# Kernel tuning notes

Measured on AMD Instinct MI355X. Metric: run time of the kernel, lower is better.

## Reference

```python
import jax, jax.numpy as jnp
import numpy as np

B = 131072
SD, AD, HID = 24, 8, 32
NH = SD + AD            # n_heads = 32
UNITS = HID * NH        # 1024


def _xavier(k, shape):
    fan_in, fan_out = shape[-2], shape[-1]
    lim = float(np.sqrt(6.0 / (fan_in + fan_out)))
    return jax.random.uniform(k, shape, jnp.float32, -lim, lim)


def setup_inputs() -> dict:
    key = jax.random.key(0)
    ks = jax.random.split(key, 8)
    return dict(
        state=jax.random.normal(ks[0], (B, SD), jnp.float32),
        action=jax.random.normal(ks[1], (B, AD), jnp.float32),
        # ripple layer 1: per-head Linear(NH -> HID), gate logits init 0 (init_prob=0.5)
        W1=_xavier(ks[2], (NH, NH, HID)), b1=jnp.zeros((NH, HID), jnp.float32), g1=jnp.zeros((NH,), jnp.float32),
        # ripple layer 2: per-head Linear(UNITS -> HID)
        W2=_xavier(ks[3], (NH, UNITS, HID)), b2=jnp.zeros((NH, HID), jnp.float32), g2=jnp.zeros((NH,), jnp.float32),
        # q_network
        Wq1=_xavier(ks[4], (UNITS, 256)), bq1=jnp.zeros((256,), jnp.float32),
        ln1_g=jnp.ones((256,), jnp.float32), ln1_b=jnp.zeros((256,), jnp.float32),
        Wq2=_xavier(ks[5], (256, 128)), bq2=jnp.zeros((128,), jnp.float32),
        ln2_g=jnp.ones((128,), jnp.float32), ln2_b=jnp.zeros((128,), jnp.float32),
        Wq3=_xavier(ks[6], (128, 1)), bq3=jnp.zeros((1,), jnp.float32),
    )


def _ripple(x, W, b, g):
    # x: [B, D]; W: [H, D, K]; per-head linear + tanh, scaled by per-head sigmoid gate
    h = jnp.tanh(jnp.einsum('bd,hdk->bhk', x, W) + b[None])  # [B, H, K]
    h = h * jax.nn.sigmoid(g)[None, :, None]
    return h.reshape(x.shape[0], -1)  # [B, H*K]


def _ln(x, g, b, eps=1e-5):
    mu = jnp.mean(x, -1, keepdims=True)
    var = jnp.mean((x - mu) ** 2, -1, keepdims=True)
    return (x - mu) * jax.lax.rsqrt(var + eps) * g + b


def reference(state, action, W1, b1, g1, W2, b2, g2,
              Wq1, bq1, ln1_g, ln1_b, Wq2, bq2, ln2_g, ln2_b, Wq3, bq3):
    sa = jnp.concatenate([state, action], axis=1)          # [B, SD+AD]
    x = _ripple(sa, W1, b1, g1)                            # [B, UNITS]
    x = _ripple(x, W2, b2, g2)                             # [B, UNITS]
    h = jax.nn.relu(_ln(x @ Wq1 + bq1, ln1_g, ln1_b))      # [B, 256] (dropout = eval identity)
    h = jax.nn.relu(_ln(h @ Wq2 + bq2, ln2_g, ln2_b))      # [B, 128]
    return h @ Wq3 + bq3                                   # [B, 1]
```

## Files before the change

kernel.cpp:

```cpp
#include <hip/hip_runtime.h>
#include <hip/hip_bf16.h>

typedef _Float16 f16x8 __attribute__((ext_vector_type(8)));
typedef _Float16 f16x4 __attribute__((ext_vector_type(4)));
typedef float f32x4 __attribute__((ext_vector_type(4)));

__device__ __forceinline__ float tanh_fast(float x) {
  float e = __expf(2.0f * x);
  return 1.0f - 2.0f * __builtin_amdgcn_rcpf(e + 1.0f);
}
__device__ __forceinline__ float sigmoid_fast(float x) {
  return __builtin_amdgcn_rcpf(1.0f + __expf(-x));
}

__global__ __launch_bounds__(256) void prep_weights(
    const float* __restrict__ W1, const float* __restrict__ W2,
    const float* __restrict__ Wq1, const float* __restrict__ Wq2,
    _Float16* __restrict__ V1p, _Float16* __restrict__ V2p,
    _Float16* __restrict__ T1p, _Float16* __restrict__ T2p) {
  __shared__ float S[32 * 33];
  int b = blockIdx.x, t = threadIdx.x;
  if (b < 2624) {
    const float* in; _Float16* out; int N, nc0, tile;
    if (b < 2048) {
      int h = b >> 6, rem = b & 63, ntl = rem >> 5, kt = rem & 31;
      in = W2 + (size_t)h * 32768 + (size_t)kt * 32 * 32;
      N = 32; nc0 = ntl * 16;
      out = V2p; tile = kt * 64 + (h * 2 + ntl);
    } else if (b < 2560) {
      int i = b - 2048, nt = i >> 5, kt = i & 31;
      in = Wq1 + (size_t)kt * 32 * 256; N = 256; nc0 = nt * 16;
      out = T1p; tile = kt * 16 + nt;
    } else {
      int i = b - 2560, nt = i >> 3, kt = i & 7;
      in = Wq2 + (size_t)kt * 32 * 128; N = 128; nc0 = nt * 16;
      out = T2p; tile = nt * 8 + kt;
    }
    if (t < 128) {
      int r = t >> 2, c4 = (t & 3) * 4;
      const float4 v = *(const float4*)(in + (size_t)r * N + nc0 + c4);
      S[r * 17 + c4 + 0] = v.x; S[r * 17 + c4 + 1] = v.y;
      S[r * 17 + c4 + 2] = v.z; S[r * 17 + c4 + 3] = v.w;
    }
    __syncthreads();
    if (t < 128) {
      int w2 = t >> 6, l = t & 63, q = l >> 4, l15 = l & 15;
      f16x4 o;
#pragma unroll
      for (int jj = 0; jj < 4; ++jj)
        o[jj] = (_Float16)S[(q * 8 + w2 * 4 + jj) * 17 + l15];
      *(f16x4*)(out + (size_t)tile * 512 + l * 8 + w2 * 4) = o;
    }
  } else {
    int h = b - 2624;
    const float* in = W1 + h * 1024;
    int cc = t & 31, rr8 = t >> 5;
#pragma unroll
    for (int p = 0; p < 4; ++p) {
      int r = rr8 + p * 8;
      S[cc * 33 + r] = in[r * 32 + cc];
    }
    __syncthreads();
    if (t < 128) {
      int ntl = t >> 6, l = t & 63, q = l >> 4, l15 = l & 15;
      f16x8 o;
#pragma unroll
      for (int j = 0; j < 8; ++j)
        o[j] = (_Float16)S[(ntl * 16 + l15) * 33 + q * 8 + j];
      *(f16x8*)(V1p + (size_t)(h * 2 + ntl) * 512 + l * 8) = o;
    }
  }
}

__global__ __launch_bounds__(512, 2) void k12_fused(
    const float* __restrict__ state, const float* __restrict__ action,
    const _Float16* __restrict__ v1p, const float* __restrict__ b1,
    const float* __restrict__ g1,
    const _Float16* __restrict__ v2p, const float* __restrict__ b2,
    const float* __restrict__ g2,
    _Float16* __restrict__ x2p, int gro, int NRT) {
  __shared__ __align__(16) _Float16 SA[128 * 40];
  __shared__ __align__(16) _Float16 XF[2 * 16384];
  __shared__ __align__(16) _Float16 EP[8 * 64 * 36];
  int g = blockIdx.x;
  int bn = g & 1, bm = g >> 1;
  int t = threadIdx.x, w = t >> 6, l = t & 63, q = l >> 4, l15 = l & 15;
  int wrow = w & 1;
  int cg = w >> 1;
  int m0 = bm * 128;

  {
    int r = t >> 2, q4 = t & 3;
    size_t grow = (size_t)(gro + m0 + r);
    float v[8];
    if (q4 < 3) {
      const float4* sp = (const float4*)(state + grow * 24 + q4 * 8);
      ((float4*)v)[0] = sp[0]; ((float4*)v)[1] = sp[1];
    } else {
      const float4* ap = (const float4*)(action + grow * 8);
      ((float4*)v)[0] = ap[0]; ((float4*)v)[1] = ap[1];
    }
    f16x8 h0;
#pragma unroll
    for (int j = 0; j < 8; ++j) h0[j] = (_Float16)v[j];
    *(f16x8*)&SA[r * 40 + q4 * 8] = h0;
  }
  __syncthreads();

  f32x4 acc[4][8] = {};
  _Float16* EPw = EP + w * (64 * 36);

  f16x8 rb[2];
#pragma unroll
  for (int ni = 0; ni < 2; ++ni)
    rb[ni] = *(const f16x8*)(v1p + (size_t)(cg * 2 + ni) * 512 + l * 8);

  const int nt0 = bn * 32 + cg * 8;
  const _Float16* bBase = v2p + (size_t)nt0 * 512 + (size_t)l * 8;

  for (int kc = 0; kc < 8; ++kc) {
    f16x8 asa[4];
#pragma unroll
    for (int mi = 0; mi < 4; ++mi)
      asa[mi] = *(const f16x8*)&SA[(wrow * 64 + mi * 16 + l15) * 40 + q * 8];
    f32x4 a1[4][2] = {};
#pragma unroll
    for (int mi = 0; mi < 4; ++mi)
#pragma unroll
      for (int ni = 0; ni < 2; ++ni)
        a1[mi][ni] = __builtin_amdgcn_mfma_f32_16x16x32_f16(asa[mi], rb[ni], a1[mi][ni], 0, 0, 0);
#pragma unroll
    for (int ni = 0; ni < 2; ++ni) {
      int col = kc * 128 + cg * 32 + ni * 16 + l15;
      float sg = sigmoid_fast(g1[col >> 5]);
      float bias = b1[col];
#pragma unroll
      for (int mi = 0; mi < 4; ++mi)
#pragma unroll
        for (int r = 0; r < 4; ++r)
          EPw[(mi * 16 + q * 4 + r) * 36 + ni * 16 + l15] =
              (_Float16)(tanh_fast(a1[mi][ni][r] + bias) * sg);
    }
    _Float16* buf = XF + (kc & 1) * 16384;
#pragma unroll
    for (int rtl = 0; rtl < 4; ++rtl) {
      int base = (rtl * 16 + l15) * 36 + q * 8;
      union { f16x8 v; f16x4 h[2]; } u;
      u.h[0] = *(const f16x4*)&EPw[base];
      u.h[1] = *(const f16x4*)&EPw[base + 4];
      *(f16x8*)(buf + ((cg * 8 + wrow * 4 + rtl) * 64 + l) * 8) = u.v;
    }
    __syncthreads();

    if (kc < 7) {
#pragma unroll
      for (int ni = 0; ni < 2; ++ni)
        rb[ni] = *(const f16x8*)(v1p + (size_t)((kc + 1) * 8 + cg * 2 + ni) * 512 + l * 8);
    }
    int ktg = kc * 4;
    f16x8 bb0[8], bb1[8];
#pragma unroll
    for (int ni = 0; ni < 8; ++ni)
      bb0[ni] = *(const f16x8*)(bBase + (size_t)(ktg * 64 + ni) * 512);
#pragma unroll
    for (int ni = 0; ni < 8; ++ni)
      bb1[ni] = *(const f16x8*)(bBase + (size_t)((ktg + 1) * 64 + ni) * 512);
#pragma unroll
    for (int ktL = 0; ktL < 4; ++ktL) {
      f16x8 af[4];
#pragma unroll
      for (int mi = 0; mi < 4; ++mi)
        af[mi] = *(const f16x8*)(buf + ((ktL * 8 + wrow * 4 + mi) * 64 + l) * 8);
      f16x8* bb = (ktL & 1) ? bb1 : bb0;
#pragma unroll
      for (int mi = 0; mi < 4; ++mi)
#pragma unroll
        for (int ni = 0; ni < 8; ++ni)
          acc[mi][ni] = __builtin_amdgcn_mfma_f32_16x16x32_f16(af[mi], bb[ni], acc[mi][ni], 0, 0, 0);
      if (ktL == 0) {
#pragma unroll
        for (int ni = 0; ni < 8; ++ni)
          bb0[ni] = *(const f16x8*)(bBase + (size_t)((ktg + 2) * 64 + ni) * 512);
      } else if (ktL == 1) {
#pragma unroll
        for (int ni = 0; ni < 8; ++ni)
          bb1[ni] = *(const f16x8*)(bBase + (size_t)((ktg + 3) * 64 + ni) * 512);
      }
    }
  }

  for (int kcg = 0; kcg < 4; ++kcg) {
#pragma unroll
    for (int np = 0; np < 2; ++np) {
      int ni = kcg * 2 + np;
      int col = (nt0 + ni) * 16 + l15;
      float sg = sigmoid_fast(g2[col >> 5]);
      float bias = b2[col];
#pragma unroll
      for (int mi = 0; mi < 4; ++mi)
#pragma unroll
        for (int r = 0; r < 4; ++r)
          EPw[(mi * 16 + q * 4 + r) * 36 + np * 16 + l15] =
              (_Float16)(tanh_fast(acc[mi][ni][r] + bias) * sg);
    }
#pragma unroll
    for (int rtl = 0; rtl < 4; ++rtl) {
      int base = (rtl * 16 + l15) * 36 + q * 8;
      union { f16x8 v; f16x4 h[2]; } u;
      u.h[0] = *(const f16x4*)&EPw[base];
      u.h[1] = *(const f16x4*)&EPw[base + 4];
      int kc2 = (nt0 >> 1) + kcg;
      int rt = bm * 8 + wrow * 4 + rtl;
      *(f16x8*)(x2p + ((size_t)kc2 * NRT + rt) * 512 + l * 8) = u.v;
    }
  }
}

__global__ __launch_bounds__(512, 3) void k3_head(
    const _Float16* __restrict__ x2p, const _Float16* __restrict__ t1p,
    const _Float16* __restrict__ t2p,
    const float* __restrict__ bq1, const float* __restrict__ ln1g, const float* __restrict__ ln1b,
    const float* __restrict__ bq2, const float* __restrict__ ln2g, const float* __restrict__ ln2b,
    const float* __restrict__ wq3, const float* __restrict__ bq3,
    float* __restrict__ out, int NRT, int SROWS) {
  __shared__ __align__(16) _Float16 y1h[128 * 264];
  __shared__ float redA[128 * 4], redB[128 * 4];
  __shared__ float meanv[128], rstdv[128];
  int bm = blockIdx.x;
  int t = threadIdx.x, w = t >> 6, l = t & 63, q = l >> 4, l15 = l & 15;
  int wr = w >> 2, wc = w & 3;

  int gt = bm * 8;
  int slice = 0;
  if (gt >= NRT) { slice = 1; gt -= NRT; }
  int rt0 = gt + wr * 4;

  f32x4 acc[4][4] = {};
  const size_t aStep = (size_t)NRT * 512;
  const _Float16* aP = x2p + (size_t)slice * SROWS * 1024 + (size_t)rt0 * 512 + (size_t)l * 8;
  const _Float16* bP = t1p + (size_t)(wc * 4) * 512 + (size_t)l * 8;

  f16x8 a0[4], a1[4], b0[4], b1[4];
#pragma unroll
  for (int mi = 0; mi < 4; ++mi) a0[mi] = *(const f16x8*)(aP + mi * 512);
#pragma unroll
  for (int ni = 0; ni < 4; ++ni) b0[ni] = *(const f16x8*)(bP + ni * 512);
#pragma unroll
  for (int mi = 0; mi < 4; ++mi) a1[mi] = *(const f16x8*)(aP + aStep + mi * 512);
#pragma unroll
  for (int ni = 0; ni < 4; ++ni) b1[ni] = *(const f16x8*)(bP + 8192 + ni * 512);
  aP += 2 * aStep; bP += 16384;

  for (int kt = 0; kt < 32; kt += 2) {
#pragma unroll
    for (int mi = 0; mi < 4; ++mi)
#pragma unroll
      for (int ni = 0; ni < 4; ++ni)
        acc[mi][ni] = __builtin_amdgcn_mfma_f32_16x16x32_f16(a0[mi], b0[ni], acc[mi][ni], 0, 0, 0);
    if (kt < 30) {
#pragma unroll
      for (int mi = 0; mi < 4; ++mi) a0[mi] = *(const f16x8*)(aP + mi * 512);
#pragma unroll
      for (int ni = 0; ni < 4; ++ni) b0[ni] = *(const f16x8*)(bP + ni * 512);
    }
#pragma unroll
    for (int mi = 0; mi < 4; ++mi)
#pragma unroll
      for (int ni = 0; ni < 4; ++ni)
        acc[mi][ni] = __builtin_amdgcn_mfma_f32_16x16x32_f16(a1[mi], b1[ni], acc[mi][ni], 0, 0, 0);
    if (kt < 30) {
#pragma unroll
      for (int mi = 0; mi < 4; ++mi) a1[mi] = *(const f16x8*)(aP + aStep + mi * 512);
#pragma unroll
      for (int ni = 0; ni < 4; ++ni) b1[ni] = *(const f16x8*)(bP + 8192 + ni * 512);
      aP += 2 * aStep; bP += 16384;
    }
  }

#pragma unroll
  for (int ni = 0; ni < 4; ++ni) {
    int col = wc * 64 + ni * 16 + l15;
    float b = bq1[col];
#pragma unroll
    for (int mi = 0; mi < 4; ++mi)
#pragma unroll
      for (int r = 0; r < 4; ++r) acc[mi][ni][r] += b;
  }
#pragma unroll
  for (int mi = 0; mi < 4; ++mi)
#pragma unroll
    for (int r = 0; r < 4; ++r) {
      int row = wr * 64 + mi * 16 + q * 4 + r;
      float s = 0.f, sq = 0.f;
#pragma unroll
      for (int ni = 0; ni < 4; ++ni) { float v = acc[mi][ni][r]; s += v; sq += v * v; }
#pragma unroll
      for (int off = 1; off < 16; off <<= 1) { s += __shfl_xor(s, off); sq += __shfl_xor(sq, off); }
      if (l15 == 0) { redA[row * 4 + wc] = s; redB[row * 4 + wc] = sq; }
    }
  __syncthreads();
  if (t < 128) {
    float s  = redA[t * 4] + redA[t * 4 + 1] + redA[t * 4 + 2] + redA[t * 4 + 3];
    float sq = redB[t * 4] + redB[t * 4 + 1] + redB[t * 4 + 2] + redB[t * 4 + 3];
    float mean = s * (1.0f / 256.0f);
    float var = sq * (1.0f / 256.0f) - mean * mean;
    meanv[t] = mean; rstdv[t] = rsqrtf(var + 1e-5f);
  }
  __syncthreads();
#pragma unroll
  for (int mi = 0; mi < 4; ++mi)
#pragma unroll
    for (int ni = 0; ni < 4; ++ni)
#pragma unroll
      for (int r = 0; r < 4; ++r) {
        int row = wr * 64 + mi * 16 + q * 4 + r;
        int col = wc * 64 + ni * 16 + l15;
        float y = (acc[mi][ni][r] - meanv[row]) * rstdv[row] * ln1g[col] + ln1b[col];
        y = fmaxf(y, 0.f);
        y1h[row * 264 + col] = (_Float16)y;
      }
  __syncthreads();

  f32x4 a2[4][2] = {};
  for (int kt = 0; kt < 8; ++kt) {
    f16x8 af2[4];
#pragma unroll
    for (int mi = 0; mi < 4; ++mi)
      af2[mi] = *(const f16x8*)&y1h[(wr * 64 + mi * 16 + l15) * 264 + kt * 32 + q * 8];
#pragma unroll
    for (int ni = 0; ni < 2; ++ni) {
      f16x8 bf = *(const f16x8*)(t2p + (size_t)(wc * 2 + ni) * 4096 + kt * 512 + l * 8);
#pragma unroll
      for (int mi = 0; mi < 4; ++mi)
        a2[mi][ni] = __builtin_amdgcn_mfma_f32_16x16x32_f16(af2[mi], bf, a2[mi][ni], 0, 0, 0);
    }
  }
#pragma unroll
  for (int ni = 0; ni < 2; ++ni) {
    int col = wc * 32 + ni * 16 + l15;
    float b = bq2[col];
#pragma unroll
    for (int mi = 0; mi < 4; ++mi)
#pragma unroll
      for (int r = 0; r < 4; ++r) a2[mi][ni][r] += b;
  }
  __syncthreads();
#pragma unroll
  for (int mi = 0; mi < 4; ++mi)
#pragma unroll
    for (int r = 0; r < 4; ++r) {
      int row = wr * 64 + mi * 16 + q * 4 + r;
      float s = 0.f, sq = 0.f;
#pragma unroll
      for (int ni = 0; ni < 2; ++ni) { float v = a2[mi][ni][r]; s += v; sq += v * v; }
#pragma unroll
      for (int off = 1; off < 16; off <<= 1) { s += __shfl_xor(s, off); sq += __shfl_xor(sq, off); }
      if (l15 == 0) { redA[row * 4 + wc] = s; redB[row * 4 + wc] = sq; }
    }
  __syncthreads();
  if (t < 128) {
    float s  = redA[t * 4] + redA[t * 4 + 1] + redA[t * 4 + 2] + redA[t * 4 + 3];
    float sq = redB[t * 4] + redB[t * 4 + 1] + redB[t * 4 + 2] + redB[t * 4 + 3];
    float mean = s * (1.0f / 128.0f);
    float var = sq * (1.0f / 128.0f) - mean * mean;
    meanv[t] = mean; rstdv[t] = rsqrtf(var + 1e-5f);
  }
  __syncthreads();
#pragma unroll
  for (int mi = 0; mi < 4; ++mi)
#pragma unroll
    for (int r = 0; r < 4; ++r) {
      int row = wr * 64 + mi * 16 + q * 4 + r;
      float pr = 0.f;
#pragma unroll
      for (int ni = 0; ni < 2; ++ni) {
        int col = wc * 32 + ni * 16 + l15;
        float y = (a2[mi][ni][r] - meanv[row]) * rstdv[row] * ln2g[col] + ln2b[col];
        y = fmaxf(y, 0.f);
        pr += y * wq3[col];
      }
#pragma unroll
      for (int off = 1; off < 16; off <<= 1) pr += __shfl_xor(pr, off);
      if (l15 == 0) redA[row * 4 + wc] = pr;
    }
  __syncthreads();
  if (t < 128)
    out[bm * 128 + t] = redA[t * 4] + redA[t * 4 + 1] + redA[t * 4 + 2] + redA[t * 4 + 3] + bq3[0];
}

extern "C" void kernel_launch(void* const* d_in, const int* in_sizes, int n_in,
                              void* d_out, int out_size, void* d_ws, size_t ws_size,
                              hipStream_t stream) {
  const float* state  = (const float*)d_in[0];
  const float* action = (const float*)d_in[1];
  const float* W1  = (const float*)d_in[2];
  const float* b1  = (const float*)d_in[3];
  const float* g1  = (const float*)d_in[4];
  const float* W2  = (const float*)d_in[5];
  const float* b2  = (const float*)d_in[6];
  const float* g2  = (const float*)d_in[7];
  const float* Wq1 = (const float*)d_in[8];
  const float* bq1 = (const float*)d_in[9];
  const float* ln1g = (const float*)d_in[10];
  const float* ln1b = (const float*)d_in[11];
  const float* Wq2 = (const float*)d_in[12];
  const float* bq2 = (const float*)d_in[13];
  const float* ln2g = (const float*)d_in[14];
  const float* ln2b = (const float*)d_in[15];
  const float* Wq3 = (const float*)d_in[16];
  const float* bq3 = (const float*)d_in[17];
  int B = in_sizes[0] / 24;

  char* ws = (char*)d_ws;
  _Float16* V1p = (_Float16*)(ws);
  _Float16* V2p = (_Float16*)(ws + 65536);
  _Float16* T1p = (_Float16*)(ws + 65536 + 2097152);
  _Float16* T2p = (_Float16*)(ws + 65536 + 2097152 + 524288);
  size_t woff = (65536 + 2097152 + 524288 + 65536 + 4095) & ~(size_t)4095;

  size_t avail = ws_size > woff ? ws_size - woff : 0;
  int S, G;
  if (avail >= (size_t)32768 * 2048 * 2) {
    S = 32768; G = 2;
  } else {
    long rows = (long)(avail / 2048);
    if (rows > 32768) rows = 32768;
    rows &= ~127L;
    if (rows < 128) rows = 128;
    S = (int)rows; G = 1;
  }
  _Float16* x2 = (_Float16*)(ws + woff);
  int NRT = S / 16;

  prep_weights<<<2656, 256, 0, stream>>>(W1, W2, Wq1, Wq2, V1p, V2p, T1p, T2p);

  int nsl = (B + S - 1) / S;
  for (int i = 0; i < nsl; ++i) {
    int r0 = i * S;
    int Sc = S < (B - r0) ? S : (B - r0);
    int nbm = Sc / 128;
    k12_fused<<<dim3(2 * nbm), 512, 0, stream>>>(state, action, V1p, b1, g1,
                                                 V2p, b2, g2,
                                                 x2 + (size_t)(i % G) * S * 1024, r0, NRT);
    if (i % G == G - 1 || i == nsl - 1) {
      int gstart = (i - i % G) * S;
      int nrows = r0 + Sc - gstart;
      k3_head<<<dim3(nrows / 128), 512, 0, stream>>>(x2, T1p, T2p, bq1, ln1g, ln1b,
                                                     bq2, ln2g, ln2b, Wq3, bq3,
                                                     (float*)d_out + gstart, NRT, S);
    }
  }
}
```

Baseline: 608.5 us.

## Swap MFMA operand order to write epilogue fragments directly, dropping EP staging

Swaps the MFMA A/B operands so each lane's accumulator holds four consecutive K indices of one row. This lets tanh/gate epilogue results be packed straight into f16x8 operand fragments, with no LDS transpose through a staging buffer. The weight prep kernel permutes K order within the V2p and T1p tiles to match the new fragment layout. The EP shared buffer is removed, which shrinks LDS use and cuts LDS round trips. The SA fragments are also hoisted out of the kc loop. This depends on the K permutation being consistent between producer and consumer, including in the unseen k3_head for T1p.

```diff
diff --git a/kernel.cpp b/kernel.cpp
--- a/kernel.cpp
+++ b/kernel.cpp
@@ -21,20 +21,20 @@
   __shared__ float S[32 * 33];
   int b = blockIdx.x, t = threadIdx.x;
   if (b < 2624) {
-    const float* in; _Float16* out; int N, nc0, tile;
+    const float* in; _Float16* out; int N, nc0, tile, use_pi;
     if (b < 2048) {
       int h = b >> 6, rem = b & 63, ntl = rem >> 5, kt = rem & 31;
       in = W2 + (size_t)h * 32768 + (size_t)kt * 32 * 32;
       N = 32; nc0 = ntl * 16;
-      out = V2p; tile = kt * 64 + (h * 2 + ntl);
+      out = V2p; tile = kt * 64 + (h * 2 + ntl); use_pi = 1;
     } else if (b < 2560) {
       int i = b - 2048, nt = i >> 5, kt = i & 31;
       in = Wq1 + (size_t)kt * 32 * 256; N = 256; nc0 = nt * 16;
-      out = T1p; tile = kt * 16 + nt;
+      out = T1p; tile = kt * 16 + nt; use_pi = 1;
     } else {
       int i = b - 2560, nt = i >> 3, kt = i & 7;
       in = Wq2 + (size_t)kt * 32 * 128; N = 128; nc0 = nt * 16;
-      out = T2p; tile = nt * 8 + kt;
+      out = T2p; tile = nt * 8 + kt; use_pi = 0;
     }
     if (t < 128) {
       int r = t >> 2, c4 = (t & 3) * 4;
@@ -47,8 +47,10 @@
       int w2 = t >> 6, l = t & 63, q = l >> 4, l15 = l & 15;
       f16x4 o;
 #pragma unroll
-      for (int jj = 0; jj < 4; ++jj)
-        o[jj] = (_Float16)S[(q * 8 + w2 * 4 + jj) * 17 + l15];
+      for (int jj = 0; jj < 4; ++jj) {
+        int kl = use_pi ? (q * 4 + jj + w2 * 16) : (q * 8 + w2 * 4 + jj);
+        o[jj] = (_Float16)S[kl * 17 + l15];
+      }
       *(f16x4*)(out + (size_t)tile * 512 + l * 8 + w2 * 4) = o;
     }
   } else {
@@ -81,7 +83,6 @@
     _Float16* __restrict__ x2p, int gro, int NRT) {
   __shared__ __align__(16) _Float16 SA[128 * 40];
   __shared__ __align__(16) _Float16 XF[2 * 16384];
-  __shared__ __align__(16) _Float16 EP[8 * 64 * 36];
   int g = blockIdx.x;
   int bn = g & 1, bm = g >> 1;
   int t = threadIdx.x, w = t >> 6, l = t & 63, q = l >> 4, l15 = l & 15;
@@ -107,8 +108,10 @@
   }
   __syncthreads();
 
-  f32x4 acc[4][8] = {};
-  _Float16* EPw = EP + w * (64 * 36);
+  f16x8 asa[4];
+#pragma unroll
+  for (int p = 0; p < 4; ++p)
+    asa[p] = *(const f16x8*)&SA[((wrow * 4 + p) * 16 + l15) * 40 + q * 8];
 
   f16x8 rb[2];
 #pragma unroll
@@ -117,66 +120,54 @@
 
   const int nt0 = bn * 32 + cg * 8;
   const _Float16* bBase = v2p + (size_t)nt0 * 512 + (size_t)l * 8;
+  f32x4 acc[4][8] = {};
 
   for (int kc = 0; kc < 8; ++kc) {
-    f16x8 asa[4];
-#pragma unroll
-    for (int mi = 0; mi < 4; ++mi)
-      asa[mi] = *(const f16x8*)&SA[(wrow * 64 + mi * 16 + l15) * 40 + q * 8];
-    f32x4 a1[4][2] = {};
-#pragma unroll
-    for (int mi = 0; mi < 4; ++mi)
-#pragma unroll
-      for (int ni = 0; ni < 2; ++ni)
-        a1[mi][ni] = __builtin_amdgcn_mfma_f32_16x16x32_f16(asa[mi], rb[ni], a1[mi][ni], 0, 0, 0);
-#pragma unroll
-    for (int ni = 0; ni < 2; ++ni) {
-      int col = kc * 128 + cg * 32 + ni * 16 + l15;
-      float sg = sigmoid_fast(g1[col >> 5]);
-      float bias = b1[col];
-#pragma unroll
-      for (int mi = 0; mi < 4; ++mi)
-#pragma unroll
-        for (int r = 0; r < 4; ++r)
-          EPw[(mi * 16 + q * 4 + r) * 36 + ni * 16 + l15] =
-              (_Float16)(tanh_fast(a1[mi][ni][r] + bias) * sg);
-    }
+    int ktg = kc * 4;
+    f16x8 bb0[8], bb1[8];
+#pragma unroll
+    for (int ni = 0; ni < 8; ++ni)
+      bb0[ni] = *(const f16x8*)(bBase + (size_t)(ktg * 64 + ni) * 512);
+#pragma unroll
+    for (int ni = 0; ni < 8; ++ni)
+      bb1[ni] = *(const f16x8*)(bBase + (size_t)((ktg + 1) * 64 + ni) * 512);
+
     _Float16* buf = XF + (kc & 1) * 16384;
-#pragma unroll
-    for (int rtl = 0; rtl < 4; ++rtl) {
-      int base = (rtl * 16 + l15) * 36 + q * 8;
-      union { f16x8 v; f16x4 h[2]; } u;
-      u.h[0] = *(const f16x4*)&EPw[base];
-      u.h[1] = *(const f16x4*)&EPw[base + 4];
-      *(f16x8*)(buf + ((cg * 8 + wrow * 4 + rtl) * 64 + l) * 8) = u.v;
+    float sg1 = sigmoid_fast(g1[kc * 4 + cg]);
+    f32x4 bs0 = *(const f32x4*)(b1 + kc * 128 + cg * 32 + q * 4);
+    f32x4 bs1 = *(const f32x4*)(b1 + kc * 128 + cg * 32 + 16 + q * 4);
+#pragma unroll
+    for (int p = 0; p < 4; ++p) {
+      f32x4 d0 = {}, d1 = {};
+      d0 = __builtin_amdgcn_mfma_f32_16x16x32_f16(rb[0], asa[p], d0, 0, 0, 0);
+      d1 = __builtin_amdgcn_mfma_f32_16x16x32_f16(rb[1], asa[p], d1, 0, 0, 0);
+      f16x8 o;
+#pragma unroll
+      for (int r = 0; r < 4; ++r) {
+        o[r]     = (_Float16)(tanh_fast(d0[r] + bs0[r]) * sg1);
+        o[4 + r] = (_Float16)(tanh_fast(d1[r] + bs1[r]) * sg1);
+      }
+      *(f16x8*)(buf + (size_t)(cg * 8 + wrow * 4 + p) * 512 + l * 8) = o;
     }
     __syncthreads();
-
     if (kc < 7) {
 #pragma unroll
       for (int ni = 0; ni < 2; ++ni)
         rb[ni] = *(const f16x8*)(v1p + (size_t)((kc + 1) * 8 + cg * 2 + ni) * 512 + l * 8);
     }
-    int ktg = kc * 4;
-    f16x8 bb0[8], bb1[8];
-#pragma unroll
-    for (int ni = 0; ni < 8; ++ni)
-      bb0[ni] = *(const f16x8*)(bBase + (size_t)(ktg * 64 + ni) * 512);
-#pragma unroll
-    for (int ni = 0; ni < 8; ++ni)
-      bb1[ni] = *(const f16x8*)(bBase + (size_t)((ktg + 1) * 64 + ni) * 512);
+
 #pragma unroll
     for (int ktL = 0; ktL < 4; ++ktL) {
-      f16x8 af[4];
+      f16x8 xa[4];
 #pragma unroll
       for (int mi = 0; mi < 4; ++mi)
-        af[mi] = *(const f16x8*)(buf + ((ktL * 8 + wrow * 4 + mi) * 64 + l) * 8);
+        xa[mi] = *(const f16x8*)(buf + (size_t)(ktL * 8 + wrow * 4 + mi) * 512 + l * 8);
       f16x8* bb = (ktL & 1) ? bb1 : bb0;
 #pragma unroll
       for (int mi = 0; mi < 4; ++mi)
 #pragma unroll
         for (int ni = 0; ni < 8; ++ni)
-          acc[mi][ni] = __builtin_amdgcn_mfma_f32_16x16x32_f16(af[mi], bb[ni], acc[mi][ni], 0, 0, 0);
+          acc[mi][ni] = __builtin_amdgcn_mfma_f32_16x16x32_f16(bb[ni], xa[mi], acc[mi][ni], 0, 0, 0);
       if (ktL == 0) {
 #pragma unroll
         for (int ni = 0; ni < 8; ++ni)
@@ -189,29 +180,22 @@
     }
   }
 
-  for (int kcg = 0; kcg < 4; ++kcg) {
-#pragma unroll
-    for (int np = 0; np < 2; ++np) {
-      int ni = kcg * 2 + np;
-      int col = (nt0 + ni) * 16 + l15;
-      float sg = sigmoid_fast(g2[col >> 5]);
-      float bias = b2[col];
-#pragma unroll
-      for (int mi = 0; mi < 4; ++mi)
-#pragma unroll
-        for (int r = 0; r < 4; ++r)
-          EPw[(mi * 16 + q * 4 + r) * 36 + np * 16 + l15] =
-              (_Float16)(tanh_fast(acc[mi][ni][r] + bias) * sg);
-    }
-#pragma unroll
-    for (int rtl = 0; rtl < 4; ++rtl) {
-      int base = (rtl * 16 + l15) * 36 + q * 8;
-      union { f16x8 v; f16x4 h[2]; } u;
-      u.h[0] = *(const f16x4*)&EPw[base];
-      u.h[1] = *(const f16x4*)&EPw[base + 4];
-      int kc2 = (nt0 >> 1) + kcg;
-      int rt = bm * 8 + wrow * 4 + rtl;
-      *(f16x8*)(x2p + ((size_t)kc2 * NRT + rt) * 512 + l * 8) = u.v;
+#pragma unroll
+  for (int mi = 0; mi < 4; ++mi) {
+    int rt = bm * 8 + wrow * 4 + mi;
+#pragma unroll
+    for (int p2 = 0; p2 < 4; ++p2) {
+      int kc2 = (nt0 >> 1) + p2;
+      float sg2 = sigmoid_fast(g2[kc2]);
+      f32x4 c0 = *(const f32x4*)(b2 + kc2 * 32 + q * 4);
+      f32x4 c1 = *(const f32x4*)(b2 + kc2 * 32 + 16 + q * 4);
+      f16x8 o;
+#pragma unroll
+      for (int r = 0; r < 4; ++r) {
+        o[r]     = (_Float16)(tanh_fast(acc[mi][2 * p2][r] + c0[r]) * sg2);
+        o[4 + r] = (_Float16)(tanh_fast(acc[mi][2 * p2 + 1][r] + c1[r]) * sg2);
+      }
+      *(f16x8*)(x2p + ((size_t)kc2 * NRT + rt) * 512 + l * 8) = o;
     }
   }
 }
```

Result: no change. 605.4 us (-0.5%).
